# Kernel optimization log

Measured on AMD Instinct MI355X. Metric: run time of the kernel, lower is better.

The kernel has to match this reference:

```python
import jax, jax.numpy as jnp
import numpy as np

N_BRANCHES = 4
BATCH = 8192
DIM = 4096
NUM_CLASSES = 1024
MARGIN = 0.3
EPS = 1e-8


def setup_inputs() -> dict:
    key = jax.random.key(0)
    branch_feats = jax.random.normal(key, (N_BRANCHES, BATCH, DIM), dtype=jnp.float32)
    # every class appears BATCH // NUM_CLASSES = 8 times (>1, so no detach branch)
    targets = jnp.arange(BATCH, dtype=jnp.int32) % NUM_CLASSES
    return {"branch_feats": branch_feats, "targets": targets, "num_classes": NUM_CLASSES}


def _centers(branch_feats, targets, num_classes):
    # masked per-class mean == segment mean (torch.unique over 0..C-1, sorted)
    counts = jax.ops.segment_sum(jnp.ones(branch_feats.shape[1], jnp.float32),
                                 targets, num_segments=num_classes)  # [C]
    sums = jax.vmap(lambda f: jax.ops.segment_sum(f, targets, num_segments=num_classes))(
        branch_feats)  # [N, C, D]
    return sums / counts[None, :, None]


def reference(branch_feats, targets, num_classes):
    centers = _centers(branch_feats, targets, num_classes)  # [N, C, D]
    C = num_classes

    # hard negative per (branch, class): min_{l != k} ||c[k] - c[l]||
    sq = jnp.sum(centers * centers, axis=-1)                 # [N, C]
    gram = jnp.einsum('nkd,nld->nkl', centers, centers)      # [N, C, C]
    d2 = jnp.maximum(sq[:, :, None] + sq[:, None, :] - 2.0 * gram, 0.0)
    dist = jnp.sqrt(d2)                                      # [N, C, C]
    dist = jnp.where(jnp.eye(C, dtype=bool)[None], jnp.inf, dist)
    hard_neg = jnp.min(dist, axis=-1)                        # [N, C]

    # positive distances for each unordered branch pair i < j
    ii, jj = jnp.triu_indices(N_BRANCHES, k=1)
    # F.pairwise_distance adds eps to the difference before the norm
    pos = jnp.linalg.norm(centers[ii] - centers[jj] + EPS, axis=-1)  # [P, C]

    # loss += relu(margin + pos_dist[k] - hard_neg_i[k]); valid_pairs = P * C
    return jnp.mean(jax.nn.relu(MARGIN + pos - hard_neg[ii]))
```

## Files before the change

### kernel.cpp

```cpp
#include <hip/hip_runtime.h>

#define N_BR   4
#define BATCH  8192
#define DIM    4096
#define NCLS   1024
#define MARGIN 0.3f
#define EPS_P  1e-8f
#define MAXPC  16

typedef __attribute__((ext_vector_type(4))) float f32x4;
typedef __attribute__((ext_vector_type(2))) float f32x2;
typedef __attribute__((ext_vector_type(4))) int i32x4;
typedef unsigned short u16;
typedef unsigned char u8;

__global__ __launch_bounds__(256) void centersk(
    const float* __restrict__ feats, const int* __restrict__ targets,
    u8* __restrict__ cq, float* __restrict__ sq,
    unsigned int* __restrict__ hn) {
  __shared__ int mem_s[MAXPC];
  __shared__ int cnt_s[4], off_s[5];
  __shared__ float rs[4];
  int c = blockIdx.x, n = blockIdx.y, tid = threadIdx.x;
  int w = tid >> 6, lane = tid & 63;
  if (tid == 0) hn[n * NCLS + c] = 0x7F800000u;

  int cn = 0;
  for (int i = 0; i < (BATCH / 4) / 64; ++i) {
    int b = w * (BATCH / 4) + i * 64 + lane;
    cn += __popcll(__ballot(targets[b] == c));
  }
  if (lane == 0) cnt_s[w] = cn;
  __syncthreads();
  if (tid == 0) {
    off_s[0] = 0;
    for (int i = 0; i < 4; ++i) off_s[i + 1] = off_s[i] + cnt_s[i];
  }
  __syncthreads();
  int pos = off_s[w];
  for (int i = 0; i < (BATCH / 4) / 64; ++i) {
    int b = w * (BATCH / 4) + i * 64 + lane;
    bool hit = (targets[b] == c);
    unsigned long long m = __ballot(hit);
    if (hit) {
      int p = pos + __popcll(m & ((1ULL << lane) - 1ULL));
      if (p < MAXPC) mem_s[p] = b;
    }
    pos += __popcll(m);
  }
  __syncthreads();
  int count = off_s[4]; if (count > MAXPC) count = MAXPC;
  float inv = 1.0f / (float)count;

  const float* fb = feats + (size_t)n * BATCH * DIM;
  size_t cbase = ((size_t)n * NCLS + c) * DIM;
  float ssq = 0.f;
#pragma unroll
  for (int it = 0; it < DIM / 1024; ++it) {
    int d = (it * 256 + tid) * 4;
    f32x4 acc = {0.f, 0.f, 0.f, 0.f};
    for (int m = 0; m < count; ++m) {
      int b = mem_s[m];
      f32x4 v = *(const f32x4*)(fb + (size_t)b * DIM + d);
      acc += v;
    }
    f32x4 ctr = acc * inv;
    int packed = 0;
    packed = __builtin_amdgcn_cvt_pk_fp8_f32(ctr.x, ctr.y, packed, false);
    packed = __builtin_amdgcn_cvt_pk_fp8_f32(ctr.z, ctr.w, packed, true);
    *(int*)(cq + cbase + d) = packed;
    ssq += ctr.x * ctr.x + ctr.y * ctr.y + ctr.z * ctr.z + ctr.w * ctr.w;
  }
  for (int off = 1; off < 64; off <<= 1) ssq += __shfl_xor(ssq, off, 64);
  if ((tid & 63) == 0) rs[tid >> 6] = ssq;
  __syncthreads();
  if (tid == 0) sq[n * NCLS + c] = rs[0] + rs[1] + rs[2] + rs[3];
}

__global__ __launch_bounds__(256) void gramk(
    const u8* __restrict__ cq, const float* __restrict__ sq,
    unsigned int* __restrict__ hn) {
  __shared__ u8 As[4][64 * 64];
  __shared__ u8 Bs[4][64 * 64];
  int x = (blockIdx.x & 7) * 17 + (blockIdx.x >> 3);
  int n = blockIdx.y;
  int ti = 0;
  while (x >= 16 - ti) { x -= 16 - ti; ++ti; }
  int tj = ti + x;
  int tid = threadIdx.x;
  int wid = tid >> 6, lane = tid & 63;
  int wr = wid >> 1, wc = wid & 1;
  int r0 = ti * 64, c0 = tj * 64;
  const u8* base = cq + (size_t)n * NCLS * DIM;

  f32x4 acc[2][2] = {};

#define STAGE(buf, kb)                                                          \
  {                                                                             \
    int g = tid;                              \
    int row_ = g >> 2, c16_ = g & 3;                                            \
    int sc16_ = c16_ ^ ((row_ >> 1) & 3);    \
    const u8* gA_ = base + (size_t)(r0 + row_) * DIM + (kb) + sc16_ * 16;       \
    const u8* gB_ = base + (size_t)(c0 + row_) * DIM + (kb) + sc16_ * 16;       \
    __builtin_amdgcn_global_load_lds(                                           \
        (const __attribute__((address_space(1))) void*)gA_,                     \
        (__attribute__((address_space(3))) void*)(As[buf] + g * 16), 16, 0, 0); \
    __builtin_amdgcn_global_load_lds(                                           \
        (const __attribute__((address_space(1))) void*)gB_,                     \
        (__attribute__((address_space(3))) void*)(Bs[buf] + g * 16), 16, 0, 0); \
  }

#define COMPUTE(buf)                                                            \
  {                                                                             \
    _Pragma("unroll")                                                           \
    for (int ks = 0; ks < 2; ++ks) {                                            \
      long a_[2], b_[2];                                                        \
      int co_ = ks * 4 + (lane >> 4);         \
      _Pragma("unroll")                                                         \
      for (int mi = 0; mi < 2; ++mi) {                                          \
        int r_ = wr * 32 + mi * 16 + (lane & 15);                               \
        int p_ = ((r_ >> 1) & 3) << 1;                                          \
        a_[mi] = *(const long*)(As[buf] + r_ * 64 + (co_ ^ p_) * 8);            \
      }                                                                         \
      _Pragma("unroll")                                                         \
      for (int nj = 0; nj < 2; ++nj) {                                          \
        int r_ = wc * 32 + nj * 16 + (lane & 15);                               \
        int p_ = ((r_ >> 1) & 3) << 1;                                          \
        b_[nj] = *(const long*)(Bs[buf] + r_ * 64 + (co_ ^ p_) * 8);            \
      }                                                                         \
      _Pragma("unroll")                                                         \
      for (int mi = 0; mi < 2; ++mi)                                            \
        _Pragma("unroll")                                                       \
        for (int nj = 0; nj < 2; ++nj)                                          \
          acc[mi][nj] = __builtin_amdgcn_mfma_f32_16x16x32_fp8_fp8(             \
              a_[mi], b_[nj], acc[mi][nj], 0, 0, 0);                            \
    }                                                                           \
  }

  const int NK = DIM / 64;
  STAGE(0, 0);
  STAGE(1, 64);
  STAGE(2, 128);
  for (int k = 0; k < NK; ++k) {
    if (k < NK - 2)       asm volatile("s_waitcnt vmcnt(4)" ::: "memory");
    else if (k == NK - 2) asm volatile("s_waitcnt vmcnt(2)" ::: "memory");
    else                  asm volatile("s_waitcnt vmcnt(0)" ::: "memory");
    __builtin_amdgcn_s_barrier();
    if (k + 3 < NK) STAGE((k + 3) & 3, (k + 3) * 64);
    COMPUTE(k & 3);
  }
#undef STAGE
#undef COMPUTE

  const float* sqn = sq + n * NCLS;
  unsigned int* hb = hn + n * NCLS;
  int grp = lane >> 4, lid = lane & 15;
  float d2v[2][2][4];
#pragma unroll
  for (int mi = 0; mi < 2; ++mi)
#pragma unroll
    for (int nj = 0; nj < 2; ++nj)
#pragma unroll
      for (int j = 0; j < 4; ++j) {
        int rr = r0 + wr * 32 + mi * 16 + grp * 4 + j;
        int cc = c0 + wc * 32 + nj * 16 + lid;
        float d2 = fmaxf(sqn[rr] + sqn[cc] - 2.0f * acc[mi][nj][j], 0.f);
        d2v[mi][nj][j] = (rr == cc) ? __builtin_inff() : d2;
      }
#pragma unroll
  for (int mi = 0; mi < 2; ++mi)
#pragma unroll
    for (int j = 0; j < 4; ++j) {
      float dmin = fminf(d2v[mi][0][j], d2v[mi][1][j]);
#pragma unroll
      for (int off = 1; off < 16; off <<= 1)
        dmin = fminf(dmin, __shfl_xor(dmin, off, 64));
      if (lid == 0) {
        int rr = r0 + wr * 32 + mi * 16 + grp * 4 + j;
        atomicMin(&hb[rr], __float_as_uint(dmin));
      }
    }
#pragma unroll
  for (int nj = 0; nj < 2; ++nj) {
    float cmin = __builtin_inff();
#pragma unroll
    for (int mi = 0; mi < 2; ++mi)
#pragma unroll
      for (int j = 0; j < 4; ++j)
        cmin = fminf(cmin, d2v[mi][nj][j]);
    cmin = fminf(cmin, __shfl_xor(cmin, 16, 64));
    cmin = fminf(cmin, __shfl_xor(cmin, 32, 64));
    if (grp == 0) {
      int cc = c0 + wc * 32 + nj * 16 + lid;
      atomicMin(&hb[cc], __float_as_uint(cmin));
    }
  }
}

__global__ __launch_bounds__(256) void posk(
    const u8* __restrict__ cq, const unsigned int* __restrict__ hn,
    float* __restrict__ partial) {
  int c = blockIdx.x, tid = threadIdx.x;
  const int ii[6] = {0, 0, 0, 1, 1, 2};
  const int jj[6] = {1, 2, 3, 2, 3, 3};
  float v[N_BR][16];
#pragma unroll
  for (int nb = 0; nb < N_BR; ++nb) {
    i32x4 wds = *(const i32x4*)(cq + ((size_t)nb * NCLS + c) * DIM + tid * 16);
#pragma unroll
    for (int q = 0; q < 4; ++q) {
      f32x2 lo = __builtin_amdgcn_cvt_pk_f32_fp8(wds[q], false);
      f32x2 hi = __builtin_amdgcn_cvt_pk_f32_fp8(wds[q], true);
      v[nb][q * 4 + 0] = lo.x; v[nb][q * 4 + 1] = lo.y;
      v[nb][q * 4 + 2] = hi.x; v[nb][q * 4 + 3] = hi.y;
    }
  }
  float s[6];
#pragma unroll
  for (int p = 0; p < 6; ++p) {
    float t = 0.f;
#pragma unroll
    for (int e = 0; e < 16; ++e) {
      float df = v[ii[p]][e] - v[jj[p]][e] + EPS_P;
      t += df * df;
    }
    s[p] = t;
  }
  __shared__ float red[4][6];
#pragma unroll
  for (int p = 0; p < 6; ++p) {
    float x = s[p];
    for (int off = 1; off < 64; off <<= 1) x += __shfl_xor(x, off, 64);
    if ((tid & 63) == 0) red[tid >> 6][p] = x;
  }
  __syncthreads();
  if (tid == 0) {
    float total = 0.f;
#pragma unroll
    for (int p = 0; p < 6; ++p) {
      float sum = red[0][p] + red[1][p] + red[2][p] + red[3][p];
      float pos = sqrtf(sum);
      float hneg = sqrtf(__uint_as_float(hn[ii[p] * NCLS + c]));
      float t = MARGIN + pos - hneg;
      total += fmaxf(t, 0.f);
    }
    partial[c] = total;
  }
}

__global__ void finalk(const float* __restrict__ partial, float* __restrict__ out) {
  int tid = threadIdx.x;
  float s = 0.f;
  for (int c = tid; c < NCLS; c += 256) s += partial[c];
  for (int off = 1; off < 64; off <<= 1) s += __shfl_xor(s, off, 64);
  __shared__ float rs[4];
  if ((tid & 63) == 0) rs[tid >> 6] = s;
  __syncthreads();
  if (tid == 0) out[0] = (rs[0] + rs[1] + rs[2] + rs[3]) * (1.0f / (6.0f * NCLS));
}

extern "C" void kernel_launch(void* const* d_in, const int* in_sizes, int n_in,
                              void* d_out, int out_size, void* d_ws, size_t ws_size,
                              hipStream_t stream) {
  const float* feats = (const float*)d_in[0];
  const int* targets = (const int*)d_in[1];
  float* out = (float*)d_out;
  char* ws = (char*)d_ws;

  float* sq        = (float*)(ws + 0);
  unsigned int* hn = (unsigned int*)(ws + 16384);
  float* partial   = (float*)(ws + 32768);
  u8* cq           = (u8*)(ws + 65536);

  hipLaunchKernelGGL(centersk, dim3(NCLS, N_BR), dim3(256), 0, stream,
                     feats, targets, cq, sq, hn);
  hipLaunchKernelGGL(gramk, dim3(136, N_BR), dim3(256), 0, stream, cq, sq, hn);
  hipLaunchKernelGGL(posk, dim3(NCLS), dim3(256), 0, stream, cq, hn, partial);
  hipLaunchKernelGGL(finalk, dim3(1), dim3(256), 0, stream, partial, out);
}
```

Baseline: 170.7 us.

## Split class-membership scan into prep kernel and deepen gram prefetch to six stages

```diff
diff --git a/kernel.cpp b/kernel.cpp
--- a/kernel.cpp
+++ b/kernel.cpp
@@ -11,20 +11,15 @@
 typedef __attribute__((ext_vector_type(4))) float f32x4;
 typedef __attribute__((ext_vector_type(2))) float f32x2;
 typedef __attribute__((ext_vector_type(4))) int i32x4;
-typedef unsigned short u16;
 typedef unsigned char u8;
 
-__global__ __launch_bounds__(256) void centersk(
-    const float* __restrict__ feats, const int* __restrict__ targets,
-    u8* __restrict__ cq, float* __restrict__ sq,
-    unsigned int* __restrict__ hn) {
-  __shared__ int mem_s[MAXPC];
+__global__ __launch_bounds__(256) void prepk(
+    const int* __restrict__ targets, int* __restrict__ members,
+    int* __restrict__ cnt, unsigned int* __restrict__ hn) {
   __shared__ int cnt_s[4], off_s[5];
-  __shared__ float rs[4];
-  int c = blockIdx.x, n = blockIdx.y, tid = threadIdx.x;
+  int c = blockIdx.x, tid = threadIdx.x;
   int w = tid >> 6, lane = tid & 63;
-  if (tid == 0) hn[n * NCLS + c] = 0x7F800000u;
-
+  if (tid < N_BR) hn[tid * NCLS + c] = 0x7F800000u;
   int cn = 0;
   for (int i = 0; i < (BATCH / 4) / 64; ++i) {
     int b = w * (BATCH / 4) + i * 64 + lane;
@@ -35,6 +30,7 @@
   if (tid == 0) {
     off_s[0] = 0;
     for (int i = 0; i < 4; ++i) off_s[i + 1] = off_s[i] + cnt_s[i];
+    cnt[c] = off_s[4];
   }
   __syncthreads();
   int pos = off_s[w];
@@ -44,14 +40,20 @@
     unsigned long long m = __ballot(hit);
     if (hit) {
       int p = pos + __popcll(m & ((1ULL << lane) - 1ULL));
-      if (p < MAXPC) mem_s[p] = b;
+      if (p < MAXPC) members[c * MAXPC + p] = b;
     }
     pos += __popcll(m);
   }
-  __syncthreads();
-  int count = off_s[4]; if (count > MAXPC) count = MAXPC;
+}
+
+__global__ __launch_bounds__(256) void centersk(
+    const float* __restrict__ feats, const int* __restrict__ members,
+    const int* __restrict__ cnt, u8* __restrict__ cq,
+    float* __restrict__ sq) {
+  int c = blockIdx.x, n = blockIdx.y, tid = threadIdx.x;
+  int count = cnt[c]; if (count > MAXPC) count = MAXPC;
+  int beg = c * MAXPC, end = beg + count;
   float inv = 1.0f / (float)count;
-
   const float* fb = feats + (size_t)n * BATCH * DIM;
   size_t cbase = ((size_t)n * NCLS + c) * DIM;
   float ssq = 0.f;
@@ -59,8 +61,8 @@
   for (int it = 0; it < DIM / 1024; ++it) {
     int d = (it * 256 + tid) * 4;
     f32x4 acc = {0.f, 0.f, 0.f, 0.f};
-    for (int m = 0; m < count; ++m) {
-      int b = mem_s[m];
+    for (int m = beg; m < end; ++m) {
+      int b = members[m];
       f32x4 v = *(const f32x4*)(fb + (size_t)b * DIM + d);
       acc += v;
     }
@@ -72,6 +74,7 @@
     ssq += ctr.x * ctr.x + ctr.y * ctr.y + ctr.z * ctr.z + ctr.w * ctr.w;
   }
   for (int off = 1; off < 64; off <<= 1) ssq += __shfl_xor(ssq, off, 64);
+  __shared__ float rs[4];
   if ((tid & 63) == 0) rs[tid >> 6] = ssq;
   __syncthreads();
   if (tid == 0) sq[n * NCLS + c] = rs[0] + rs[1] + rs[2] + rs[3];
@@ -80,8 +83,8 @@
 __global__ __launch_bounds__(256) void gramk(
     const u8* __restrict__ cq, const float* __restrict__ sq,
     unsigned int* __restrict__ hn) {
-  __shared__ u8 As[4][64 * 64];
-  __shared__ u8 Bs[4][64 * 64];
+  __shared__ u8 As[6][64 * 64];
+  __shared__ u8 Bs[6][64 * 64];
   int x = (blockIdx.x & 7) * 17 + (blockIdx.x >> 3);
   int n = blockIdx.y;
   int ti = 0;
@@ -138,16 +141,19 @@
   }
 
   const int NK = DIM / 64;
-  STAGE(0, 0);
-  STAGE(1, 64);
-  STAGE(2, 128);
+  STAGE(0, 0); STAGE(1, 64); STAGE(2, 128); STAGE(3, 192); STAGE(4, 256);
+  int cb = 0, sb = 5;
   for (int k = 0; k < NK; ++k) {
-    if (k < NK - 2)       asm volatile("s_waitcnt vmcnt(4)" ::: "memory");
+    if (k < NK - 4)       asm volatile("s_waitcnt vmcnt(8)" ::: "memory");
+    else if (k == NK - 4) asm volatile("s_waitcnt vmcnt(6)" ::: "memory");
+    else if (k == NK - 3) asm volatile("s_waitcnt vmcnt(4)" ::: "memory");
     else if (k == NK - 2) asm volatile("s_waitcnt vmcnt(2)" ::: "memory");
     else                  asm volatile("s_waitcnt vmcnt(0)" ::: "memory");
     __builtin_amdgcn_s_barrier();
-    if (k + 3 < NK) STAGE((k + 3) & 3, (k + 3) * 64);
-    COMPUTE(k & 3);
+    if (k + 5 < NK) STAGE(sb, (k + 5) * 64);
+    COMPUTE(cb);
+    cb = (cb == 5) ? 0 : cb + 1;
+    sb = (sb == 5) ? 0 : sb + 1;
   }
 #undef STAGE
 #undef COMPUTE
@@ -267,13 +273,17 @@
   float* out = (float*)d_out;
   char* ws = (char*)d_ws;
 
-  float* sq        = (float*)(ws + 0);
-  unsigned int* hn = (unsigned int*)(ws + 16384);
-  float* partial   = (float*)(ws + 32768);
-  u8* cq           = (u8*)(ws + 65536);
-
+  int* members     = (int*)(ws + 0);
+  int* cnt         = (int*)(ws + 65536);
+  float* sq        = (float*)(ws + 69632);
+  unsigned int* hn = (unsigned int*)(ws + 86016);
+  float* partial   = (float*)(ws + 102400);
+  u8* cq           = (u8*)(ws + 131072);
+
+  hipLaunchKernelGGL(prepk, dim3(NCLS), dim3(256), 0, stream,
+                     targets, members, cnt, hn);
   hipLaunchKernelGGL(centersk, dim3(NCLS, N_BR), dim3(256), 0, stream,
-                     feats, targets, cq, sq, hn);
+                     feats, members, cnt, cq, sq);
   hipLaunchKernelGGL(gramk, dim3(136, N_BR), dim3(256), 0, stream, cq, sq, hn);
   hipLaunchKernelGGL(posk, dim3(NCLS), dim3(256), 0, stream, cq, hn, partial);
   hipLaunchKernelGGL(finalk, dim3(1), dim3(256), 0, stream, partial, out);
```

Result: faster. 161.0 us (median of 2 runs) (-5.7%).
